# Optimization experiments

Hardware: AMD Instinct MI355X
Metric: run time of the kernel (lower is better)

The kernel has to match this reference:

```python
import jax, jax.numpy as jnp
import numpy as np

B, D, L, H = 256, 512, 64, 300


def setup_inputs() -> dict:
    key = jax.random.key(0)
    ks = jax.random.split(key, 16)
    s = 0.05  # weight init scale to keep activations sane through ReLU chains
    return {
        "x": jax.random.normal(ks[0], (B, D), jnp.float32),
        "eps": jax.random.normal(ks[1], (B, L), jnp.float32),
        "W": jax.random.normal(ks[2], (D, L), jnp.float32) * s,
        "enc1_w": jax.random.normal(ks[3], (H, D), jnp.float32) * s,
        "enc1_b": jax.random.normal(ks[4], (H,), jnp.float32) * s,
        "enc2_w": jax.random.normal(ks[5], (H, H), jnp.float32) * s,
        "enc2_b": jax.random.normal(ks[6], (H,), jnp.float32) * s,
        "zm_w": jax.random.normal(ks[7], (L, H), jnp.float32) * s,
        "zm_b": jax.random.normal(ks[8], (L,), jnp.float32) * s,
        "zv_w": jax.random.normal(ks[9], (L, H), jnp.float32) * s,
        "zv_b": jax.random.normal(ks[10], (L,), jnp.float32) * s,
        "gen1_w": jax.random.normal(ks[11], (H, L), jnp.float32) * s,
        "gen2_w": jax.random.normal(ks[12], (H, H), jnp.float32) * s,
        "gen2_b": jax.random.normal(ks[13], (H,), jnp.float32) * s,
        "head_w": jax.random.normal(ks[14], (D, H), jnp.float32) * s,
        "head_b": jax.random.normal(ks[15], (D,), jnp.float32) * s,
    }


def reference(x, eps, W, enc1_w, enc1_b, enc2_w, enc2_b, zm_w, zm_b,
              zv_w, zv_b, gen1_w, gen2_w, gen2_b, head_w, head_b):
    # encode: q_z = ReLU(Linear) -> ReLU(Linear)
    h = jax.nn.relu(x @ enc1_w.T + enc1_b)
    h = jax.nn.relu(h @ enc2_w.T + enc2_b)
    z_mean = h @ zm_w.T + zm_b          # [B, L]
    z_log_var = h @ zv_w.T + zv_b       # [B, L]
    # reparameterize (eps passed in for determinism)
    z = z_mean + eps * jnp.exp(0.5 * z_log_var)
    # decode: per-column masked z through shared generator + per-column head,
    # vectorized over the column axis D (mask = W rows)
    masked = z[:, None, :] * W[None, :, :]                       # [B, D, L]
    g1 = jax.nn.relu(jnp.einsum('bdl,hl->bdh', masked, gen1_w))  # [B, D, H]
    g2 = jax.nn.relu(jnp.einsum('bdh,gh->bdg', g1, gen2_w) + gen2_b)
    x_mean = jnp.einsum('bdh,dh->bd', g2, head_w) + head_b       # [B, D]
    return (x_mean, z, z_mean, z_log_var)
```

## Files before the change

### kernel.cpp

```cpp
#include <hip/hip_runtime.h>

typedef unsigned short u16;
typedef unsigned int u32;

typedef __bf16 bf16x8 __attribute__((ext_vector_type(8)));
typedef float f32x4 __attribute__((ext_vector_type(4)));

union V16 { uint4 u; bf16x8 v; u16 s[8]; __bf16 h[8]; };
union F4  { float4 v; float f[4]; };

__device__ __forceinline__ float bf2f(u16 a) {
  union { u32 u; float f; } c; c.u = ((u32)a) << 16; return c.f;
}

#define Z_OFF   131072
#define ZM_OFF  147456
#define ZLV_OFF 163840

#define B1_OFF 0
#define B2_OFF 2560
#define E1_OFF 15360
#define E2_OFF 35840
#define ZMP_OFF 48640
#define ZVP_OFF 51200
#define FRAG_TOTAL 53760
#define WB4  53760
#define XB4  57856
#define H1_4 74240
#define H2_4 84480
#define PACK_THREADS (FRAG_TOTAL + 4096 + 16384)

__device__ __forceinline__ void pack_one(const float* __restrict__ src,
                                         int t, int s, int lane,
                                         int Nsrc, int Ksrc, int rowlen,
                                         uint4* __restrict__ dst) {
  const int n = t * 16 + (lane & 15);
  const int k0 = s * 32 + ((lane >> 4) << 3);
  V16 v;
#pragma unroll
  for (int j = 0; j < 8; ++j) {
    const int k = k0 + j;
    v.h[j] = (n < Nsrc && k < Ksrc) ? (__bf16)src[n * rowlen + k] : (__bf16)0.f;
  }
  *dst = v.u;
}

__device__ __forceinline__ void cvt8(const float* __restrict__ src, uint4* __restrict__ dst) {
  F4 a, b; a.v = *(const float4*)src; b.v = *(const float4*)(src + 4);
  V16 v;
#pragma unroll
  for (int j = 0; j < 4; ++j) { v.h[j] = (__bf16)a.f[j]; v.h[4 + j] = (__bf16)b.f[j]; }
  *dst = v.u;
}

__global__ __launch_bounds__(256) void pack_kernel(
    const float* __restrict__ g1w, const float* __restrict__ g2w,
    const float* __restrict__ e1w, const float* __restrict__ e2w,
    const float* __restrict__ zmw, const float* __restrict__ zvw,
    const float* __restrict__ W,   const float* __restrict__ x,
    uint4* __restrict__ ws4) {
  const int idx = blockIdx.x * 256 + threadIdx.x;
  if (idx >= PACK_THREADS) return;
  const int lane = idx & 63;
  if (idx < B2_OFF) {
    const int f = (idx - B1_OFF) >> 6;
    pack_one(g1w, f >> 1, f & 1, lane, 300, 64, 64, ws4 + idx);
  } else if (idx < E1_OFF) {
    const int f = (idx - B2_OFF) >> 6;
    pack_one(g2w, f / 10, f % 10, lane, 300, 300, 300, ws4 + idx);
  } else if (idx < E2_OFF) {
    const int f = (idx - E1_OFF) >> 6;
    pack_one(e1w, f >> 4, f & 15, lane, 300, 512, 512, ws4 + idx);
  } else if (idx < ZMP_OFF) {
    const int f = (idx - E2_OFF) >> 6;
    pack_one(e2w, f / 10, f % 10, lane, 300, 300, 300, ws4 + idx);
  } else if (idx < ZVP_OFF) {
    const int f = (idx - ZMP_OFF) >> 6;
    pack_one(zmw, f / 10, f % 10, lane, 64, 300, 300, ws4 + idx);
  } else if (idx < FRAG_TOTAL) {
    const int f = (idx - ZVP_OFF) >> 6;
    pack_one(zvw, f / 10, f % 10, lane, 64, 300, 300, ws4 + idx);
  } else if (idx < FRAG_TOTAL + 4096) {
    const int i = idx - FRAG_TOTAL;
    cvt8(W + i * 8, ws4 + WB4 + i);
  } else {
    const int i = idx - FRAG_TOTAL - 4096;
    cvt8(x + i * 8, ws4 + XB4 + i);
  }
}

__global__ __launch_bounds__(64) void enc1_kernel(
    const uint4* __restrict__ xb, const uint4* __restrict__ e1p,
    const float* __restrict__ e1b, u16* __restrict__ h1) {
  const int wg = blockIdx.x;
  const int rt = wg / 20, nt = wg % 20;
  const int lane = threadIdx.x, q = lane >> 4, c = lane & 15;
  f32x4 acc = {0.f, 0.f, 0.f, 0.f};
  const int arow = rt * 16 + c;
#pragma unroll
  for (int s = 0; s < 16; ++s) {
    V16 a, b;
    a.u = xb[arow * 64 + s * 4 + q];
    b.u = e1p[(nt * 16 + s) * 64 + lane];
    acc = __builtin_amdgcn_mfma_f32_16x16x32_bf16(a.v, b.v, acc, 0, 0, 0);
  }
  const int col = nt * 16 + c;
  const float bias = (col < 300) ? e1b[col] : 0.f;
#pragma unroll
  for (int i = 0; i < 4; ++i) {
    const int row = rt * 16 + 4 * q + i;
    V16 t; t.h[0] = (col < 300) ? (__bf16)fmaxf(acc[i] + bias, 0.f) : (__bf16)0.f;
    h1[row * 320 + col] = t.s[0];
  }
}

__global__ __launch_bounds__(64) void enc2_kernel(
    const uint4* __restrict__ h1, const uint4* __restrict__ e2p,
    const float* __restrict__ e2b, u16* __restrict__ h2) {
  const int wg = blockIdx.x;
  const int rt = wg / 20, nt = wg % 20;
  const int lane = threadIdx.x, q = lane >> 4, c = lane & 15;
  f32x4 acc = {0.f, 0.f, 0.f, 0.f};
  const int arow = rt * 16 + c;
#pragma unroll
  for (int s = 0; s < 10; ++s) {
    V16 a, b;
    a.u = h1[arow * 40 + s * 4 + q];
    b.u = e2p[(nt * 10 + s) * 64 + lane];
    acc = __builtin_amdgcn_mfma_f32_16x16x32_bf16(a.v, b.v, acc, 0, 0, 0);
  }
  const int col = nt * 16 + c;
  const float bias = (col < 300) ? e2b[col] : 0.f;
#pragma unroll
  for (int i = 0; i < 4; ++i) {
    const int row = rt * 16 + 4 * q + i;
    V16 t; t.h[0] = (col < 300) ? (__bf16)fmaxf(acc[i] + bias, 0.f) : (__bf16)0.f;
    h2[row * 320 + col] = t.s[0];
  }
}

__global__ __launch_bounds__(64) void ench_kernel(
    const uint4* __restrict__ h2, const float* __restrict__ eps,
    const uint4* __restrict__ zmp, const float* __restrict__ zmb,
    const uint4* __restrict__ zvp, const float* __restrict__ zvb,
    float* __restrict__ out) {
  const int wg = blockIdx.x;
  const int rt = wg >> 2, t = wg & 3;
  const int lane = threadIdx.x, q = lane >> 4, c = lane & 15;
  f32x4 am = {0.f, 0.f, 0.f, 0.f}, av = {0.f, 0.f, 0.f, 0.f};
  const int arow = rt * 16 + c;
#pragma unroll
  for (int s = 0; s < 10; ++s) {
    V16 a, bm, bv;
    a.u = h2[arow * 40 + s * 4 + q];
    bm.u = zmp[(t * 10 + s) * 64 + lane];
    bv.u = zvp[(t * 10 + s) * 64 + lane];
    am = __builtin_amdgcn_mfma_f32_16x16x32_bf16(a.v, bm.v, am, 0, 0, 0);
    av = __builtin_amdgcn_mfma_f32_16x16x32_bf16(a.v, bv.v, av, 0, 0, 0);
  }
  const int col = t * 16 + c;
  const float bm = zmb[col], bv = zvb[col];
#pragma unroll
  for (int i = 0; i < 4; ++i) {
    const int gi = (rt * 16 + 4 * q + i) * 64 + col;
    const float zm = am[i] + bm;
    const float zlv = av[i] + bv;
    out[ZM_OFF + gi] = zm;
    out[ZLV_OFF + gi] = zlv;
    out[Z_OFF + gi] = zm + eps[gi] * expf(0.5f * zlv);
  }
}

__global__ __launch_bounds__(320, 4) void dec_kernel(
    const float* __restrict__ z,
    const uint4* __restrict__ Wb,
    const uint4* __restrict__ b1p,
    const uint4* __restrict__ b2p,
    const float* __restrict__ g2b,
    const float* __restrict__ hw,
    const float* __restrict__ hb,
    float* __restrict__ xout) {
  __shared__ u16 g1s[32 * 328];
  float* xredf = (float*)g1s;

  const int wg = blockIdx.x;
  const int r0 = wg << 5;
  const int bi = wg >> 4;
  const int d0 = r0 & 511;
  const int tid = threadIdx.x;
  const int u = tid >> 6;
  const int lane = tid & 63;
  const int q = lane >> 4;
  const int c = lane & 15;

  const float* zrow = z + bi * 64;

  bf16x8 bz[4][2];
#pragma unroll
  for (int kf = 0; kf < 2; ++kf) {
    F4 z0, z1;
    z0.v = *(const float4*)(zrow + kf * 32 + q * 8);
    z1.v = *(const float4*)(zrow + kf * 32 + q * 8 + 4);
#pragma unroll
    for (int tt = 0; tt < 4; ++tt) {
      V16 r; r.u = b1p[((4 * u + tt) * 2 + kf) * 64 + lane];
      V16 m;
#pragma unroll
      for (int j = 0; j < 4; ++j) {
        m.h[j]     = (__bf16)(bf2f(r.s[j])     * z0.f[j]);
        m.h[4 + j] = (__bf16)(bf2f(r.s[4 + j]) * z1.f[j]);
      }
      bz[tt][kf] = m.v;
    }
  }
#pragma unroll
  for (int rt = 0; rt < 2; ++rt) {
    const int rowA = rt * 16 + c;
    V16 af0, af1;
    af0.u = Wb[(d0 + rowA) * 8 + q];
    af1.u = Wb[(d0 + rowA) * 8 + 4 + q];
    f32x4 acc[4];
#pragma unroll
    for (int tt = 0; tt < 4; ++tt) acc[tt] = {0.f, 0.f, 0.f, 0.f};
#pragma unroll
    for (int tt = 0; tt < 4; ++tt) {
      acc[tt] = __builtin_amdgcn_mfma_f32_16x16x32_bf16(af0.v, bz[tt][0], acc[tt], 0, 0, 0);
      acc[tt] = __builtin_amdgcn_mfma_f32_16x16x32_bf16(af1.v, bz[tt][1], acc[tt], 0, 0, 0);
    }
    const int rwb = rt * 16 + 4 * q;
#pragma unroll
    for (int tt = 0; tt < 4; ++tt) {
      const int colb = (4 * u + tt) * 16 + c;
#pragma unroll
      for (int i = 0; i < 4; ++i) {
        V16 t; t.h[0] = (__bf16)fmaxf(acc[tt][i], 0.f);
        g1s[(rwb + i) * 328 + colb] = t.s[0];
      }
    }
  }
  __syncthreads();

  f32x4 a3[4][2];
#pragma unroll
  for (int tt = 0; tt < 4; ++tt)
#pragma unroll
    for (int rt = 0; rt < 2; ++rt) a3[tt][rt] = {0.f, 0.f, 0.f, 0.f};
  for (int s = 0; s < 10; ++s) {
    V16 b[4];
#pragma unroll
    for (int tt = 0; tt < 4; ++tt) b[tt].u = b2p[((4 * u + tt) * 10 + s) * 64 + lane];
#pragma unroll
    for (int rt = 0; rt < 2; ++rt) {
      V16 a; a.u = *(const uint4*)&g1s[(rt * 16 + c) * 328 + s * 32 + q * 8];
#pragma unroll
      for (int tt = 0; tt < 4; ++tt)
        a3[tt][rt] = __builtin_amdgcn_mfma_f32_16x16x32_bf16(a.v, b[tt].v, a3[tt][rt], 0, 0, 0);
    }
  }
  float xacc[2][4];
#pragma unroll
  for (int rt = 0; rt < 2; ++rt)
#pragma unroll
    for (int i = 0; i < 4; ++i) xacc[rt][i] = 0.f;
#pragma unroll
  for (int tt = 0; tt < 4; ++tt) {
    const int col = (4 * u + tt) * 16 + c;
    const bool inb = (col < 300);
    const float bias = inb ? g2b[col] : 0.f;
#pragma unroll
    for (int rt = 0; rt < 2; ++rt)
#pragma unroll
      for (int i = 0; i < 4; ++i) {
        const float g2v = fmaxf(a3[tt][rt][i] + bias, 0.f);
        const float h = inb ? hw[(d0 + rt * 16 + 4 * q + i) * 300 + col] : 0.f;
        xacc[rt][i] += g2v * h;
      }
  }
#pragma unroll
  for (int rt = 0; rt < 2; ++rt)
#pragma unroll
    for (int i = 0; i < 4; ++i) {
      float t = xacc[rt][i];
      t += __shfl_xor(t, 1);
      t += __shfl_xor(t, 2);
      t += __shfl_xor(t, 4);
      t += __shfl_xor(t, 8);
      xacc[rt][i] = t;
    }
  __syncthreads();
  if (c < 4) {
#pragma unroll
    for (int rt = 0; rt < 2; ++rt) {
      float t = xacc[rt][0];
      t = (c == 1) ? xacc[rt][1] : t;
      t = (c == 2) ? xacc[rt][2] : t;
      t = (c == 3) ? xacc[rt][3] : t;
      xredf[u * 32 + rt * 16 + 4 * q + c] = t;
    }
  }
  __syncthreads();
  if (tid < 32) {
    float t = hb[d0 + tid];
#pragma unroll
    for (int uu = 0; uu < 5; ++uu) t += xredf[uu * 32 + tid];
    xout[r0 + tid] = t;
  }
}

extern "C" void kernel_launch(void* const* d_in, const int* in_sizes, int n_in,
                              void* d_out, int out_size, void* d_ws, size_t ws_size,
                              hipStream_t stream) {
  const float* x   = (const float*)d_in[0];
  const float* eps = (const float*)d_in[1];
  const float* W   = (const float*)d_in[2];
  const float* e1w = (const float*)d_in[3];
  const float* e1b = (const float*)d_in[4];
  const float* e2w = (const float*)d_in[5];
  const float* e2b = (const float*)d_in[6];
  const float* zmw = (const float*)d_in[7];
  const float* zmb = (const float*)d_in[8];
  const float* zvw = (const float*)d_in[9];
  const float* zvb = (const float*)d_in[10];
  const float* g1w = (const float*)d_in[11];
  const float* g2w = (const float*)d_in[12];
  const float* g2b = (const float*)d_in[13];
  const float* hw  = (const float*)d_in[14];
  const float* hb  = (const float*)d_in[15];
  float* out = (float*)d_out;
  uint4* ws4 = (uint4*)d_ws;

  pack_kernel<<<(PACK_THREADS + 255) / 256, 256, 0, stream>>>(
      g1w, g2w, e1w, e2w, zmw, zvw, W, x, ws4);
  enc1_kernel<<<320, 64, 0, stream>>>(ws4 + XB4, ws4 + E1_OFF, e1b, (u16*)(ws4 + H1_4));
  enc2_kernel<<<320, 64, 0, stream>>>(ws4 + H1_4, ws4 + E2_OFF, e2b, (u16*)(ws4 + H2_4));
  ench_kernel<<<64, 64, 0, stream>>>(ws4 + H2_4, eps,
                                     ws4 + ZMP_OFF, zmb, ws4 + ZVP_OFF, zvb, out);
  dec_kernel<<<4096, 320, 0, stream>>>(out + Z_OFF, ws4 + WB4,
                                       ws4 + B1_OFF, ws4 + B2_OFF,
                                       g2b, hw, hb, out);
}
```

Before: 164.3 us.

## Fuse packing and encoder stages into one prep kernel; prefetch decoder B fragments

Merges the pack, enc1, enc2 and latent-head kernels into a single prep kernel. Sixteen workgroups run the whole encoder chain per 16-row batch tile, keeping h1/h2 in shared memory and converting weight fragments on the fly from fp32. The remaining workgroups pack only the decoder weights and W. In the decoder, gen2 B fragments are double-buffered and head weights are loaded before the MMA loop, with the occupancy hint lowered from 4 to 3 to make room for the extra registers. This removes three launches and the global round-trips for h1/h2, but encoder weights are now re-read and converted by each of the 16 workgroups, and the encoder runs on only 16 workgroups.

```diff
diff --git a/kernel.cpp b/kernel.cpp
--- a/kernel.cpp
+++ b/kernel.cpp
@@ -19,16 +19,10 @@
 
 #define B1_OFF 0
 #define B2_OFF 2560
-#define E1_OFF 15360
-#define E2_OFF 35840
-#define ZMP_OFF 48640
-#define ZVP_OFF 51200
-#define FRAG_TOTAL 53760
-#define WB4  53760
-#define XB4  57856
-#define H1_4 74240
-#define H2_4 84480
-#define PACK_THREADS (FRAG_TOTAL + 4096 + 16384)
+#define WB4    15360
+#define PACK_ITEMS 19456
+#define ENC_WGS 16
+#define PREP_WGS (ENC_WGS + PACK_ITEMS / 256)
 
 __device__ __forceinline__ void pack_one(const float* __restrict__ src,
                                          int t, int s, int lane,
@@ -53,116 +47,134 @@
   *dst = v.u;
 }
 
-__global__ __launch_bounds__(256) void pack_kernel(
+__device__ __forceinline__ bf16x8 bfrag(const float* __restrict__ src,
+                                        int n, int k0, int Nsrc, int Ksrc,
+                                        int rowlen) {
+  V16 m;
+  if (n < Nsrc && k0 + 8 <= Ksrc) {
+    F4 a, b;
+    a.v = *(const float4*)(src + n * rowlen + k0);
+    b.v = *(const float4*)(src + n * rowlen + k0 + 4);
+#pragma unroll
+    for (int j = 0; j < 4; ++j) { m.h[j] = (__bf16)a.f[j]; m.h[4 + j] = (__bf16)b.f[j]; }
+  } else if (n < Nsrc) {
+#pragma unroll
+    for (int j = 0; j < 8; ++j) {
+      const int k = k0 + j;
+      m.h[j] = (k < Ksrc) ? (__bf16)src[n * rowlen + k] : (__bf16)0.f;
+    }
+  } else {
+#pragma unroll
+    for (int j = 0; j < 8; ++j) m.h[j] = (__bf16)0.f;
+  }
+  return m.v;
+}
+
+__global__ __launch_bounds__(256, 2) void prep_kernel(
+    const float* __restrict__ x, const float* __restrict__ eps,
+    const float* __restrict__ e1w, const float* __restrict__ e1b,
+    const float* __restrict__ e2w, const float* __restrict__ e2b,
+    const float* __restrict__ zmw, const float* __restrict__ zmb,
+    const float* __restrict__ zvw, const float* __restrict__ zvb,
     const float* __restrict__ g1w, const float* __restrict__ g2w,
-    const float* __restrict__ e1w, const float* __restrict__ e2w,
-    const float* __restrict__ zmw, const float* __restrict__ zvw,
-    const float* __restrict__ W,   const float* __restrict__ x,
-    uint4* __restrict__ ws4) {
-  const int idx = blockIdx.x * 256 + threadIdx.x;
-  if (idx >= PACK_THREADS) return;
-  const int lane = idx & 63;
-  if (idx < B2_OFF) {
-    const int f = (idx - B1_OFF) >> 6;
-    pack_one(g1w, f >> 1, f & 1, lane, 300, 64, 64, ws4 + idx);
-  } else if (idx < E1_OFF) {
-    const int f = (idx - B2_OFF) >> 6;
-    pack_one(g2w, f / 10, f % 10, lane, 300, 300, 300, ws4 + idx);
-  } else if (idx < E2_OFF) {
-    const int f = (idx - E1_OFF) >> 6;
-    pack_one(e1w, f >> 4, f & 15, lane, 300, 512, 512, ws4 + idx);
-  } else if (idx < ZMP_OFF) {
-    const int f = (idx - E2_OFF) >> 6;
-    pack_one(e2w, f / 10, f % 10, lane, 300, 300, 300, ws4 + idx);
-  } else if (idx < ZVP_OFF) {
-    const int f = (idx - ZMP_OFF) >> 6;
-    pack_one(zmw, f / 10, f % 10, lane, 64, 300, 300, ws4 + idx);
-  } else if (idx < FRAG_TOTAL) {
-    const int f = (idx - ZVP_OFF) >> 6;
-    pack_one(zvw, f / 10, f % 10, lane, 64, 300, 300, ws4 + idx);
-  } else if (idx < FRAG_TOTAL + 4096) {
-    const int i = idx - FRAG_TOTAL;
-    cvt8(W + i * 8, ws4 + WB4 + i);
-  } else {
-    const int i = idx - FRAG_TOTAL - 4096;
-    cvt8(x + i * 8, ws4 + XB4 + i);
-  }
-}
-
-__global__ __launch_bounds__(64) void enc1_kernel(
-    const uint4* __restrict__ xb, const uint4* __restrict__ e1p,
-    const float* __restrict__ e1b, u16* __restrict__ h1) {
-  const int wg = blockIdx.x;
-  const int rt = wg / 20, nt = wg % 20;
-  const int lane = threadIdx.x, q = lane >> 4, c = lane & 15;
-  f32x4 acc = {0.f, 0.f, 0.f, 0.f};
-  const int arow = rt * 16 + c;
+    const float* __restrict__ W,
+    uint4* __restrict__ ws4, float* __restrict__ out) {
+  if (blockIdx.x >= ENC_WGS) {
+    const int idx = (blockIdx.x - ENC_WGS) * 256 + threadIdx.x;
+    const int lane = idx & 63;
+    if (idx < B2_OFF) {
+      const int f = idx >> 6;
+      pack_one(g1w, f >> 1, f & 1, lane, 300, 64, 64, ws4 + idx);
+    } else if (idx < WB4) {
+      const int f = (idx - B2_OFF) >> 6;
+      pack_one(g2w, f / 10, f % 10, lane, 300, 300, 300, ws4 + idx);
+    } else {
+      const int i = idx - WB4;
+      cvt8(W + i * 8, ws4 + WB4 + i);
+    }
+    return;
+  }
+
+  __shared__ u16 h1s[16 * 328];
+  __shared__ u16 h2s[16 * 328];
+  const int bi0 = blockIdx.x * 16;
+  const int tid = threadIdx.x;
+  const int w = tid >> 6, lane = tid & 63, q = lane >> 4, c = lane & 15;
+
+  bf16x8 af[16];
 #pragma unroll
   for (int s = 0; s < 16; ++s) {
-    V16 a, b;
-    a.u = xb[arow * 64 + s * 4 + q];
-    b.u = e1p[(nt * 16 + s) * 64 + lane];
-    acc = __builtin_amdgcn_mfma_f32_16x16x32_bf16(a.v, b.v, acc, 0, 0, 0);
-  }
-  const int col = nt * 16 + c;
-  const float bias = (col < 300) ? e1b[col] : 0.f;
+    const float* px = x + (bi0 + c) * 512 + s * 32 + q * 8;
+    F4 a, b; a.v = *(const float4*)px; b.v = *(const float4*)(px + 4);
+    V16 m;
+#pragma unroll
+    for (int j = 0; j < 4; ++j) { m.h[j] = (__bf16)a.f[j]; m.h[4 + j] = (__bf16)b.f[j]; }
+    af[s] = m.v;
+  }
+  f32x4 acc[5];
+#pragma unroll
+  for (int tt = 0; tt < 5; ++tt) acc[tt] = {0.f, 0.f, 0.f, 0.f};
+#pragma unroll
+  for (int s = 0; s < 16; ++s) {
+    const int k0 = s * 32 + q * 8;
+#pragma unroll
+    for (int tt = 0; tt < 5; ++tt) {
+      const int n = (w * 5 + tt) * 16 + c;
+      bf16x8 b = bfrag(e1w, n, k0, 300, 512, 512);
+      acc[tt] = __builtin_amdgcn_mfma_f32_16x16x32_bf16(af[s], b, acc[tt], 0, 0, 0);
+    }
+  }
+#pragma unroll
+  for (int tt = 0; tt < 5; ++tt) {
+    const int col = (w * 5 + tt) * 16 + c;
+    const float bias = (col < 300) ? e1b[col] : 0.f;
+#pragma unroll
+    for (int i = 0; i < 4; ++i) {
+      V16 t; t.h[0] = (col < 300) ? (__bf16)fmaxf(acc[tt][i] + bias, 0.f) : (__bf16)0.f;
+      h1s[(4 * q + i) * 328 + col] = t.s[0];
+    }
+  }
+  __syncthreads();
+#pragma unroll
+  for (int tt = 0; tt < 5; ++tt) acc[tt] = {0.f, 0.f, 0.f, 0.f};
+#pragma unroll
+  for (int s = 0; s < 10; ++s) {
+    V16 a; a.u = *(const uint4*)&h1s[c * 328 + s * 32 + q * 8];
+    const int k0 = s * 32 + q * 8;
+#pragma unroll
+    for (int tt = 0; tt < 5; ++tt) {
+      const int n = (w * 5 + tt) * 16 + c;
+      bf16x8 b = bfrag(e2w, n, k0, 300, 300, 300);
+      acc[tt] = __builtin_amdgcn_mfma_f32_16x16x32_bf16(a.v, b, acc[tt], 0, 0, 0);
+    }
+  }
+#pragma unroll
+  for (int tt = 0; tt < 5; ++tt) {
+    const int col = (w * 5 + tt) * 16 + c;
+    const float bias = (col < 300) ? e2b[col] : 0.f;
+#pragma unroll
+    for (int i = 0; i < 4; ++i) {
+      V16 t; t.h[0] = (col < 300) ? (__bf16)fmaxf(acc[tt][i] + bias, 0.f) : (__bf16)0.f;
+      h2s[(4 * q + i) * 328 + col] = t.s[0];
+    }
+  }
+  __syncthreads();
+  f32x4 am = {0.f, 0.f, 0.f, 0.f}, av = {0.f, 0.f, 0.f, 0.f};
+#pragma unroll
+  for (int s = 0; s < 10; ++s) {
+    V16 a; a.u = *(const uint4*)&h2s[c * 328 + s * 32 + q * 8];
+    const int k0 = s * 32 + q * 8;
+    const int n = w * 16 + c;
+    bf16x8 bm = bfrag(zmw, n, k0, 64, 300, 300);
+    bf16x8 bv = bfrag(zvw, n, k0, 64, 300, 300);
+    am = __builtin_amdgcn_mfma_f32_16x16x32_bf16(a.v, bm, am, 0, 0, 0);
+    av = __builtin_amdgcn_mfma_f32_16x16x32_bf16(a.v, bv, av, 0, 0, 0);
+  }
+  const int col = w * 16 + c;
+  const float bm = zmb[col], bv = zvb[col];
 #pragma unroll
   for (int i = 0; i < 4; ++i) {
-    const int row = rt * 16 + 4 * q + i;
-    V16 t; t.h[0] = (col < 300) ? (__bf16)fmaxf(acc[i] + bias, 0.f) : (__bf16)0.f;
-    h1[row * 320 + col] = t.s[0];
-  }
-}
-
-__global__ __launch_bounds__(64) void enc2_kernel(
-    const uint4* __restrict__ h1, const uint4* __restrict__ e2p,
-    const float* __restrict__ e2b, u16* __restrict__ h2) {
-  const int wg = blockIdx.x;
-  const int rt = wg / 20, nt = wg % 20;
-  const int lane = threadIdx.x, q = lane >> 4, c = lane & 15;
-  f32x4 acc = {0.f, 0.f, 0.f, 0.f};
-  const int arow = rt * 16 + c;
-#pragma unroll
-  for (int s = 0; s < 10; ++s) {
-    V16 a, b;
-    a.u = h1[arow * 40 + s * 4 + q];
-    b.u = e2p[(nt * 10 + s) * 64 + lane];
-    acc = __builtin_amdgcn_mfma_f32_16x16x32_bf16(a.v, b.v, acc, 0, 0, 0);
-  }
-  const int col = nt * 16 + c;
-  const float bias = (col < 300) ? e2b[col] : 0.f;
-#pragma unroll
-  for (int i = 0; i < 4; ++i) {
-    const int row = rt * 16 + 4 * q + i;
-    V16 t; t.h[0] = (col < 300) ? (__bf16)fmaxf(acc[i] + bias, 0.f) : (__bf16)0.f;
-    h2[row * 320 + col] = t.s[0];
-  }
-}
-
-__global__ __launch_bounds__(64) void ench_kernel(
-    const uint4* __restrict__ h2, const float* __restrict__ eps,
-    const uint4* __restrict__ zmp, const float* __restrict__ zmb,
-    const uint4* __restrict__ zvp, const float* __restrict__ zvb,
-    float* __restrict__ out) {
-  const int wg = blockIdx.x;
-  const int rt = wg >> 2, t = wg & 3;
-  const int lane = threadIdx.x, q = lane >> 4, c = lane & 15;
-  f32x4 am = {0.f, 0.f, 0.f, 0.f}, av = {0.f, 0.f, 0.f, 0.f};
-  const int arow = rt * 16 + c;
-#pragma unroll
-  for (int s = 0; s < 10; ++s) {
-    V16 a, bm, bv;
-    a.u = h2[arow * 40 + s * 4 + q];
-    bm.u = zmp[(t * 10 + s) * 64 + lane];
-    bv.u = zvp[(t * 10 + s) * 64 + lane];
-    am = __builtin_amdgcn_mfma_f32_16x16x32_bf16(a.v, bm.v, am, 0, 0, 0);
-    av = __builtin_amdgcn_mfma_f32_16x16x32_bf16(a.v, bv.v, av, 0, 0, 0);
-  }
-  const int col = t * 16 + c;
-  const float bm = zmb[col], bv = zvb[col];
-#pragma unroll
-  for (int i = 0; i < 4; ++i) {
-    const int gi = (rt * 16 + 4 * q + i) * 64 + col;
+    const int gi = (bi0 + 4 * q + i) * 64 + col;
     const float zm = am[i] + bm;
     const float zlv = av[i] + bv;
     out[ZM_OFF + gi] = zm;
@@ -171,7 +183,7 @@
   }
 }
 
-__global__ __launch_bounds__(320, 4) void dec_kernel(
+__global__ __launch_bounds__(320, 3) void dec_kernel(
     const float* __restrict__ z,
     const uint4* __restrict__ Wb,
     const uint4* __restrict__ b1p,
@@ -240,42 +252,57 @@
   }
   __syncthreads();
 
-  f32x4 a3[4][2];
-#pragma unroll
-  for (int tt = 0; tt < 4; ++tt)
-#pragma unroll
-    for (int rt = 0; rt < 2; ++rt) a3[tt][rt] = {0.f, 0.f, 0.f, 0.f};
-  for (int s = 0; s < 10; ++s) {
-    V16 b[4];
-#pragma unroll
-    for (int tt = 0; tt < 4; ++tt) b[tt].u = b2p[((4 * u + tt) * 10 + s) * 64 + lane];
-#pragma unroll
-    for (int rt = 0; rt < 2; ++rt) {
-      V16 a; a.u = *(const uint4*)&g1s[(rt * 16 + c) * 328 + s * 32 + q * 8];
-#pragma unroll
-      for (int tt = 0; tt < 4; ++tt)
-        a3[tt][rt] = __builtin_amdgcn_mfma_f32_16x16x32_bf16(a.v, b[tt].v, a3[tt][rt], 0, 0, 0);
-    }
-  }
-  float xacc[2][4];
-#pragma unroll
-  for (int rt = 0; rt < 2; ++rt)
-#pragma unroll
-    for (int i = 0; i < 4; ++i) xacc[rt][i] = 0.f;
+  float hwv[4][2][4];
+  float bias[4];
 #pragma unroll
   for (int tt = 0; tt < 4; ++tt) {
     const int col = (4 * u + tt) * 16 + c;
     const bool inb = (col < 300);
-    const float bias = inb ? g2b[col] : 0.f;
+    bias[tt] = inb ? g2b[col] : 0.f;
 #pragma unroll
     for (int rt = 0; rt < 2; ++rt)
 #pragma unroll
-      for (int i = 0; i < 4; ++i) {
-        const float g2v = fmaxf(a3[tt][rt][i] + bias, 0.f);
-        const float h = inb ? hw[(d0 + rt * 16 + 4 * q + i) * 300 + col] : 0.f;
-        xacc[rt][i] += g2v * h;
-      }
-  }
+      for (int i = 0; i < 4; ++i)
+        hwv[tt][rt][i] = inb ? hw[(d0 + rt * 16 + 4 * q + i) * 300 + col] : 0.f;
+  }
+
+  f32x4 a3[4][2];
+#pragma unroll
+  for (int tt = 0; tt < 4; ++tt)
+#pragma unroll
+    for (int rt = 0; rt < 2; ++rt) a3[tt][rt] = {0.f, 0.f, 0.f, 0.f};
+  V16 bp[2][4];
+#pragma unroll
+  for (int tt = 0; tt < 4; ++tt) bp[0][tt].u = b2p[((4 * u + tt) * 10 + 0) * 64 + lane];
+  for (int s = 0; s < 10; ++s) {
+    const int cur = s & 1, nxt = cur ^ 1;
+    if (s < 9) {
+#pragma unroll
+      for (int tt = 0; tt < 4; ++tt)
+        bp[nxt][tt].u = b2p[((4 * u + tt) * 10 + s + 1) * 64 + lane];
+    }
+#pragma unroll
+    for (int rt = 0; rt < 2; ++rt) {
+      V16 a; a.u = *(const uint4*)&g1s[(rt * 16 + c) * 328 + s * 32 + q * 8];
+#pragma unroll
+      for (int tt = 0; tt < 4; ++tt)
+        a3[tt][rt] = __builtin_amdgcn_mfma_f32_16x16x32_bf16(a.v, bp[cur][tt].v, a3[tt][rt], 0, 0, 0);
+    }
+  }
+
+  float xacc[2][4];
+#pragma unroll
+  for (int rt = 0; rt < 2; ++rt)
+#pragma unroll
+    for (int i = 0; i < 4; ++i) xacc[rt][i] = 0.f;
+#pragma unroll
+  for (int tt = 0; tt < 4; ++tt)
+#pragma unroll
+    for (int rt = 0; rt < 2; ++rt)
+#pragma unroll
+      for (int i = 0; i < 4; ++i)
+        xacc[rt][i] += fmaxf(a3[tt][rt][i] + bias[tt], 0.f) * hwv[tt][rt][i];
+
 #pragma unroll
   for (int rt = 0; rt < 2; ++rt)
 #pragma unroll
@@ -329,12 +356,9 @@
   float* out = (float*)d_out;
   uint4* ws4 = (uint4*)d_ws;
 
-  pack_kernel<<<(PACK_THREADS + 255) / 256, 256, 0, stream>>>(
-      g1w, g2w, e1w, e2w, zmw, zvw, W, x, ws4);
-  enc1_kernel<<<320, 64, 0, stream>>>(ws4 + XB4, ws4 + E1_OFF, e1b, (u16*)(ws4 + H1_4));
-  enc2_kernel<<<320, 64, 0, stream>>>(ws4 + H1_4, ws4 + E2_OFF, e2b, (u16*)(ws4 + H2_4));
-  ench_kernel<<<64, 64, 0, stream>>>(ws4 + H2_4, eps,
-                                     ws4 + ZMP_OFF, zmb, ws4 + ZVP_OFF, zvb, out);
+  prep_kernel<<<PREP_WGS, 256, 0, stream>>>(x, eps, e1w, e1b, e2w, e2b,
+                                            zmw, zmb, zvw, zvb, g1w, g2w, W,
+                                            ws4, out);
   dec_kernel<<<4096, 320, 0, stream>>>(out + Z_OFF, ws4 + WB4,
                                        ws4 + B1_OFF, ws4 + B2_OFF,
                                        g2b, hw, hb, out);
```

New measurement: 221.4 us. +34.8%, slower.

## Fuse all stages into one persistent kernel with software grid barriers

Applied to the files above, without the earlier changes.

Replaces the five separate launches (pack, enc1, enc2, latent head, decoder) with one persistent kernel of 512 workgroups. Stages are separated by an atomic-counter grid barrier, and the decoder loops over its 4096 tiles. The goal is to remove launch gaps and tail effects between the small encoder kernels. In exchange the grid must be fully co-resident for the spin barrier to avoid deadlock, a memset is added each call, and the small stages now run on only a fraction of the grid while the rest wait.

```diff
diff --git a/kernel.cpp b/kernel.cpp
--- a/kernel.cpp
+++ b/kernel.cpp
@@ -28,7 +28,10 @@
 #define XB4  57856
 #define H1_4 74240
 #define H2_4 84480
-#define PACK_THREADS (FRAG_TOTAL + 4096 + 16384)
+#define PACK_ITEMS 74240
+#define BAR_U4 94720
+#define NWG 512
+#define NTHR 320
 
 __device__ __forceinline__ void pack_one(const float* __restrict__ src,
                                          int t, int s, int lane,
@@ -53,257 +56,277 @@
   *dst = v.u;
 }
 
-__global__ __launch_bounds__(256) void pack_kernel(
+__device__ __forceinline__ void gbar(u32* bar, u32 target, int tid) {
+  __syncthreads();
+  if (tid == 0) {
+    __threadfence();
+    __hip_atomic_fetch_add(bar, 1u, __ATOMIC_RELEASE, __HIP_MEMORY_SCOPE_AGENT);
+    u32 v;
+    do {
+      __builtin_amdgcn_s_sleep(4);
+      v = __hip_atomic_load(bar, __ATOMIC_ACQUIRE, __HIP_MEMORY_SCOPE_AGENT);
+    } while (v < target);
+  }
+  __syncthreads();
+}
+
+__global__ __launch_bounds__(NTHR, 4) void fused_kernel(
+    const float* __restrict__ x, const float* __restrict__ eps,
+    const float* __restrict__ e1w, const float* __restrict__ e1b,
+    const float* __restrict__ e2w, const float* __restrict__ e2b,
+    const float* __restrict__ zmw, const float* __restrict__ zmb,
+    const float* __restrict__ zvw, const float* __restrict__ zvb,
     const float* __restrict__ g1w, const float* __restrict__ g2w,
-    const float* __restrict__ e1w, const float* __restrict__ e2w,
-    const float* __restrict__ zmw, const float* __restrict__ zvw,
-    const float* __restrict__ W,   const float* __restrict__ x,
-    uint4* __restrict__ ws4) {
-  const int idx = blockIdx.x * 256 + threadIdx.x;
-  if (idx >= PACK_THREADS) return;
-  const int lane = idx & 63;
-  if (idx < B2_OFF) {
-    const int f = (idx - B1_OFF) >> 6;
-    pack_one(g1w, f >> 1, f & 1, lane, 300, 64, 64, ws4 + idx);
-  } else if (idx < E1_OFF) {
-    const int f = (idx - B2_OFF) >> 6;
-    pack_one(g2w, f / 10, f % 10, lane, 300, 300, 300, ws4 + idx);
-  } else if (idx < E2_OFF) {
-    const int f = (idx - E1_OFF) >> 6;
-    pack_one(e1w, f >> 4, f & 15, lane, 300, 512, 512, ws4 + idx);
-  } else if (idx < ZMP_OFF) {
-    const int f = (idx - E2_OFF) >> 6;
-    pack_one(e2w, f / 10, f % 10, lane, 300, 300, 300, ws4 + idx);
-  } else if (idx < ZVP_OFF) {
-    const int f = (idx - ZMP_OFF) >> 6;
-    pack_one(zmw, f / 10, f % 10, lane, 64, 300, 300, ws4 + idx);
-  } else if (idx < FRAG_TOTAL) {
-    const int f = (idx - ZVP_OFF) >> 6;
-    pack_one(zvw, f / 10, f % 10, lane, 64, 300, 300, ws4 + idx);
-  } else if (idx < FRAG_TOTAL + 4096) {
-    const int i = idx - FRAG_TOTAL;
-    cvt8(W + i * 8, ws4 + WB4 + i);
-  } else {
-    const int i = idx - FRAG_TOTAL - 4096;
-    cvt8(x + i * 8, ws4 + XB4 + i);
-  }
-}
-
-__global__ __launch_bounds__(64) void enc1_kernel(
-    const uint4* __restrict__ xb, const uint4* __restrict__ e1p,
-    const float* __restrict__ e1b, u16* __restrict__ h1) {
-  const int wg = blockIdx.x;
-  const int rt = wg / 20, nt = wg % 20;
-  const int lane = threadIdx.x, q = lane >> 4, c = lane & 15;
-  f32x4 acc = {0.f, 0.f, 0.f, 0.f};
-  const int arow = rt * 16 + c;
-#pragma unroll
-  for (int s = 0; s < 16; ++s) {
-    V16 a, b;
-    a.u = xb[arow * 64 + s * 4 + q];
-    b.u = e1p[(nt * 16 + s) * 64 + lane];
-    acc = __builtin_amdgcn_mfma_f32_16x16x32_bf16(a.v, b.v, acc, 0, 0, 0);
-  }
-  const int col = nt * 16 + c;
-  const float bias = (col < 300) ? e1b[col] : 0.f;
-#pragma unroll
-  for (int i = 0; i < 4; ++i) {
-    const int row = rt * 16 + 4 * q + i;
-    V16 t; t.h[0] = (col < 300) ? (__bf16)fmaxf(acc[i] + bias, 0.f) : (__bf16)0.f;
-    h1[row * 320 + col] = t.s[0];
-  }
-}
-
-__global__ __launch_bounds__(64) void enc2_kernel(
-    const uint4* __restrict__ h1, const uint4* __restrict__ e2p,
-    const float* __restrict__ e2b, u16* __restrict__ h2) {
-  const int wg = blockIdx.x;
-  const int rt = wg / 20, nt = wg % 20;
-  const int lane = threadIdx.x, q = lane >> 4, c = lane & 15;
-  f32x4 acc = {0.f, 0.f, 0.f, 0.f};
-  const int arow = rt * 16 + c;
-#pragma unroll
-  for (int s = 0; s < 10; ++s) {
-    V16 a, b;
-    a.u = h1[arow * 40 + s * 4 + q];
-    b.u = e2p[(nt * 10 + s) * 64 + lane];
-    acc = __builtin_amdgcn_mfma_f32_16x16x32_bf16(a.v, b.v, acc, 0, 0, 0);
-  }
-  const int col = nt * 16 + c;
-  const float bias = (col < 300) ? e2b[col] : 0.f;
-#pragma unroll
-  for (int i = 0; i < 4; ++i) {
-    const int row = rt * 16 + 4 * q + i;
-    V16 t; t.h[0] = (col < 300) ? (__bf16)fmaxf(acc[i] + bias, 0.f) : (__bf16)0.f;
-    h2[row * 320 + col] = t.s[0];
-  }
-}
-
-__global__ __launch_bounds__(64) void ench_kernel(
-    const uint4* __restrict__ h2, const float* __restrict__ eps,
-    const uint4* __restrict__ zmp, const float* __restrict__ zmb,
-    const uint4* __restrict__ zvp, const float* __restrict__ zvb,
-    float* __restrict__ out) {
-  const int wg = blockIdx.x;
-  const int rt = wg >> 2, t = wg & 3;
-  const int lane = threadIdx.x, q = lane >> 4, c = lane & 15;
-  f32x4 am = {0.f, 0.f, 0.f, 0.f}, av = {0.f, 0.f, 0.f, 0.f};
-  const int arow = rt * 16 + c;
-#pragma unroll
-  for (int s = 0; s < 10; ++s) {
-    V16 a, bm, bv;
-    a.u = h2[arow * 40 + s * 4 + q];
-    bm.u = zmp[(t * 10 + s) * 64 + lane];
-    bv.u = zvp[(t * 10 + s) * 64 + lane];
-    am = __builtin_amdgcn_mfma_f32_16x16x32_bf16(a.v, bm.v, am, 0, 0, 0);
-    av = __builtin_amdgcn_mfma_f32_16x16x32_bf16(a.v, bv.v, av, 0, 0, 0);
-  }
-  const int col = t * 16 + c;
-  const float bm = zmb[col], bv = zvb[col];
-#pragma unroll
-  for (int i = 0; i < 4; ++i) {
-    const int gi = (rt * 16 + 4 * q + i) * 64 + col;
-    const float zm = am[i] + bm;
-    const float zlv = av[i] + bv;
-    out[ZM_OFF + gi] = zm;
-    out[ZLV_OFF + gi] = zlv;
-    out[Z_OFF + gi] = zm + eps[gi] * expf(0.5f * zlv);
-  }
-}
-
-__global__ __launch_bounds__(320, 4) void dec_kernel(
-    const float* __restrict__ z,
-    const uint4* __restrict__ Wb,
-    const uint4* __restrict__ b1p,
-    const uint4* __restrict__ b2p,
-    const float* __restrict__ g2b,
-    const float* __restrict__ hw,
-    const float* __restrict__ hb,
-    float* __restrict__ xout) {
+    const float* __restrict__ g2b, const float* __restrict__ hw,
+    const float* __restrict__ hb, const float* __restrict__ W,
+    uint4* __restrict__ ws4, float* __restrict__ out) {
   __shared__ u16 g1s[32 * 328];
   float* xredf = (float*)g1s;
 
-  const int wg = blockIdx.x;
-  const int r0 = wg << 5;
-  const int bi = wg >> 4;
-  const int d0 = r0 & 511;
+  u32* bar = (u32*)(ws4 + BAR_U4);
+  const int wgid = blockIdx.x;
   const int tid = threadIdx.x;
-  const int u = tid >> 6;
   const int lane = tid & 63;
   const int q = lane >> 4;
   const int c = lane & 15;
-
-  const float* zrow = z + bi * 64;
-
-  bf16x8 bz[4][2];
-#pragma unroll
-  for (int kf = 0; kf < 2; ++kf) {
-    F4 z0, z1;
-    z0.v = *(const float4*)(zrow + kf * 32 + q * 8);
-    z1.v = *(const float4*)(zrow + kf * 32 + q * 8 + 4);
+  const int gw = wgid * 5 + (tid >> 6);
+
+  {
+    const int idx = wgid * NTHR + tid;
+    if (idx < PACK_ITEMS) {
+      const int l = idx & 63;
+      if (idx < B2_OFF) {
+        const int f = idx >> 6;
+        pack_one(g1w, f >> 1, f & 1, l, 300, 64, 64, ws4 + idx);
+      } else if (idx < E1_OFF) {
+        const int f = (idx - B2_OFF) >> 6;
+        pack_one(g2w, f / 10, f % 10, l, 300, 300, 300, ws4 + idx);
+      } else if (idx < E2_OFF) {
+        const int f = (idx - E1_OFF) >> 6;
+        pack_one(e1w, f >> 4, f & 15, l, 300, 512, 512, ws4 + idx);
+      } else if (idx < ZMP_OFF) {
+        const int f = (idx - E2_OFF) >> 6;
+        pack_one(e2w, f / 10, f % 10, l, 300, 300, 300, ws4 + idx);
+      } else if (idx < ZVP_OFF) {
+        const int f = (idx - ZMP_OFF) >> 6;
+        pack_one(zmw, f / 10, f % 10, l, 64, 300, 300, ws4 + idx);
+      } else if (idx < FRAG_TOTAL) {
+        const int f = (idx - ZVP_OFF) >> 6;
+        pack_one(zvw, f / 10, f % 10, l, 64, 300, 300, ws4 + idx);
+      } else if (idx < XB4) {
+        const int i = idx - WB4;
+        cvt8(W + i * 8, ws4 + WB4 + i);
+      } else {
+        const int i = idx - XB4;
+        cvt8(x + i * 8, ws4 + XB4 + i);
+      }
+    }
+  }
+  gbar(bar, 1 * NWG, tid);
+
+  if (gw < 320) {
+    const uint4* xb = ws4 + XB4;
+    const uint4* e1p = ws4 + E1_OFF;
+    u16* h1 = (u16*)(ws4 + H1_4);
+    const int rt = gw / 20, nt = gw % 20;
+    f32x4 acc = {0.f, 0.f, 0.f, 0.f};
+    const int arow = rt * 16 + c;
+#pragma unroll
+    for (int s = 0; s < 16; ++s) {
+      V16 a, b;
+      a.u = xb[arow * 64 + s * 4 + q];
+      b.u = e1p[(nt * 16 + s) * 64 + lane];
+      acc = __builtin_amdgcn_mfma_f32_16x16x32_bf16(a.v, b.v, acc, 0, 0, 0);
+    }
+    const int col = nt * 16 + c;
+    const float bias = (col < 300) ? e1b[col] : 0.f;
+#pragma unroll
+    for (int i = 0; i < 4; ++i) {
+      const int row = rt * 16 + 4 * q + i;
+      V16 t; t.h[0] = (col < 300) ? (__bf16)fmaxf(acc[i] + bias, 0.f) : (__bf16)0.f;
+      h1[row * 320 + col] = t.s[0];
+    }
+  }
+  gbar(bar, 2 * NWG, tid);
+
+  if (gw < 320) {
+    const uint4* h1 = ws4 + H1_4;
+    const uint4* e2p = ws4 + E2_OFF;
+    u16* h2 = (u16*)(ws4 + H2_4);
+    const int rt = gw / 20, nt = gw % 20;
+    f32x4 acc = {0.f, 0.f, 0.f, 0.f};
+    const int arow = rt * 16 + c;
+#pragma unroll
+    for (int s = 0; s < 10; ++s) {
+      V16 a, b;
+      a.u = h1[arow * 40 + s * 4 + q];
+      b.u = e2p[(nt * 10 + s) * 64 + lane];
+      acc = __builtin_amdgcn_mfma_f32_16x16x32_bf16(a.v, b.v, acc, 0, 0, 0);
+    }
+    const int col = nt * 16 + c;
+    const float bias = (col < 300) ? e2b[col] : 0.f;
+#pragma unroll
+    for (int i = 0; i < 4; ++i) {
+      const int row = rt * 16 + 4 * q + i;
+      V16 t; t.h[0] = (col < 300) ? (__bf16)fmaxf(acc[i] + bias, 0.f) : (__bf16)0.f;
+      h2[row * 320 + col] = t.s[0];
+    }
+  }
+  gbar(bar, 3 * NWG, tid);
+
+  if (gw < 64) {
+    const uint4* h2 = ws4 + H2_4;
+    const uint4* zmp = ws4 + ZMP_OFF;
+    const uint4* zvp = ws4 + ZVP_OFF;
+    const int rt = gw >> 2, t = gw & 3;
+    f32x4 am = {0.f, 0.f, 0.f, 0.f}, av = {0.f, 0.f, 0.f, 0.f};
+    const int arow = rt * 16 + c;
+#pragma unroll
+    for (int s = 0; s < 10; ++s) {
+      V16 a, bm, bv;
+      a.u = h2[arow * 40 + s * 4 + q];
+      bm.u = zmp[(t * 10 + s) * 64 + lane];
+      bv.u = zvp[(t * 10 + s) * 64 + lane];
+      am = __builtin_amdgcn_mfma_f32_16x16x32_bf16(a.v, bm.v, am, 0, 0, 0);
+      av = __builtin_amdgcn_mfma_f32_16x16x32_bf16(a.v, bv.v, av, 0, 0, 0);
+    }
+    const int col = t * 16 + c;
+    const float bm = zmb[col], bv = zvb[col];
+#pragma unroll
+    for (int i = 0; i < 4; ++i) {
+      const int gi = (rt * 16 + 4 * q + i) * 64 + col;
+      const float zm = am[i] + bm;
+      const float zlv = av[i] + bv;
+      out[ZM_OFF + gi] = zm;
+      out[ZLV_OFF + gi] = zlv;
+      out[Z_OFF + gi] = zm + eps[gi] * expf(0.5f * zlv);
+    }
+  }
+  gbar(bar, 4 * NWG, tid);
+
+  const float* z = out + Z_OFF;
+  const uint4* Wb = ws4 + WB4;
+  const uint4* b1p = ws4 + B1_OFF;
+  const uint4* b2p = ws4 + B2_OFF;
+  const int u = tid >> 6;
+
+  for (int vt = wgid; vt < 4096; vt += NWG) {
+    const int r0 = vt << 5;
+    const int bi = vt >> 4;
+    const int d0 = r0 & 511;
+    const float* zrow = z + bi * 64;
+
+    bf16x8 bz[4][2];
+#pragma unroll
+    for (int kf = 0; kf < 2; ++kf) {
+      F4 z0, z1;
+      z0.v = *(const float4*)(zrow + kf * 32 + q * 8);
+      z1.v = *(const float4*)(zrow + kf * 32 + q * 8 + 4);
+#pragma unroll
+      for (int tt = 0; tt < 4; ++tt) {
+        V16 r; r.u = b1p[((4 * u + tt) * 2 + kf) * 64 + lane];
+        V16 m;
+#pragma unroll
+        for (int j = 0; j < 4; ++j) {
+          m.h[j]     = (__bf16)(bf2f(r.s[j])     * z0.f[j]);
+          m.h[4 + j] = (__bf16)(bf2f(r.s[4 + j]) * z1.f[j]);
+        }
+        bz[tt][kf] = m.v;
+      }
+    }
+#pragma unroll
+    for (int rt = 0; rt < 2; ++rt) {
+      const int rowA = rt * 16 + c;
+      V16 af0, af1;
+      af0.u = Wb[(d0 + rowA) * 8 + q];
+      af1.u = Wb[(d0 + rowA) * 8 + 4 + q];
+      f32x4 acc[4];
+#pragma unroll
+      for (int tt = 0; tt < 4; ++tt) acc[tt] = {0.f, 0.f, 0.f, 0.f};
+#pragma unroll
+      for (int tt = 0; tt < 4; ++tt) {
+        acc[tt] = __builtin_amdgcn_mfma_f32_16x16x32_bf16(af0.v, bz[tt][0], acc[tt], 0, 0, 0);
+        acc[tt] = __builtin_amdgcn_mfma_f32_16x16x32_bf16(af1.v, bz[tt][1], acc[tt], 0, 0, 0);
+      }
+      const int rwb = rt * 16 + 4 * q;
+#pragma unroll
+      for (int tt = 0; tt < 4; ++tt) {
+        const int colb = (4 * u + tt) * 16 + c;
+#pragma unroll
+        for (int i = 0; i < 4; ++i) {
+          V16 t; t.h[0] = (__bf16)fmaxf(acc[tt][i], 0.f);
+          g1s[(rwb + i) * 328 + colb] = t.s[0];
+        }
+      }
+    }
+    __syncthreads();
+
+    f32x4 a3[4][2];
+#pragma unroll
+    for (int tt = 0; tt < 4; ++tt)
+#pragma unroll
+      for (int rt = 0; rt < 2; ++rt) a3[tt][rt] = {0.f, 0.f, 0.f, 0.f};
+    for (int s = 0; s < 10; ++s) {
+      V16 b[4];
+#pragma unroll
+      for (int tt = 0; tt < 4; ++tt) b[tt].u = b2p[((4 * u + tt) * 10 + s) * 64 + lane];
+#pragma unroll
+      for (int rt = 0; rt < 2; ++rt) {
+        V16 a; a.u = *(const uint4*)&g1s[(rt * 16 + c) * 328 + s * 32 + q * 8];
+#pragma unroll
+        for (int tt = 0; tt < 4; ++tt)
+          a3[tt][rt] = __builtin_amdgcn_mfma_f32_16x16x32_bf16(a.v, b[tt].v, a3[tt][rt], 0, 0, 0);
+      }
+    }
+    float xacc[2][4];
+#pragma unroll
+    for (int rt = 0; rt < 2; ++rt)
+#pragma unroll
+      for (int i = 0; i < 4; ++i) xacc[rt][i] = 0.f;
 #pragma unroll
     for (int tt = 0; tt < 4; ++tt) {
-      V16 r; r.u = b1p[((4 * u + tt) * 2 + kf) * 64 + lane];
-      V16 m;
-#pragma unroll
-      for (int j = 0; j < 4; ++j) {
-        m.h[j]     = (__bf16)(bf2f(r.s[j])     * z0.f[j]);
-        m.h[4 + j] = (__bf16)(bf2f(r.s[4 + j]) * z1.f[j]);
-      }
-      bz[tt][kf] = m.v;
-    }
-  }
-#pragma unroll
-  for (int rt = 0; rt < 2; ++rt) {
-    const int rowA = rt * 16 + c;
-    V16 af0, af1;
-    af0.u = Wb[(d0 + rowA) * 8 + q];
-    af1.u = Wb[(d0 + rowA) * 8 + 4 + q];
-    f32x4 acc[4];
-#pragma unroll
-    for (int tt = 0; tt < 4; ++tt) acc[tt] = {0.f, 0.f, 0.f, 0.f};
-#pragma unroll
-    for (int tt = 0; tt < 4; ++tt) {
-      acc[tt] = __builtin_amdgcn_mfma_f32_16x16x32_bf16(af0.v, bz[tt][0], acc[tt], 0, 0, 0);
-      acc[tt] = __builtin_amdgcn_mfma_f32_16x16x32_bf16(af1.v, bz[tt][1], acc[tt], 0, 0, 0);
-    }
-    const int rwb = rt * 16 + 4 * q;
-#pragma unroll
-    for (int tt = 0; tt < 4; ++tt) {
-      const int colb = (4 * u + tt) * 16 + c;
+      const int col = (4 * u + tt) * 16 + c;
+      const bool inb = (col < 300);
+      const float bias = inb ? g2b[col] : 0.f;
+#pragma unroll
+      for (int rt = 0; rt < 2; ++rt)
+#pragma unroll
+        for (int i = 0; i < 4; ++i) {
+          const float g2v = fmaxf(a3[tt][rt][i] + bias, 0.f);
+          const float h = inb ? hw[(d0 + rt * 16 + 4 * q + i) * 300 + col] : 0.f;
+          xacc[rt][i] += g2v * h;
+        }
+    }
+#pragma unroll
+    for (int rt = 0; rt < 2; ++rt)
 #pragma unroll
       for (int i = 0; i < 4; ++i) {
-        V16 t; t.h[0] = (__bf16)fmaxf(acc[tt][i], 0.f);
-        g1s[(rwb + i) * 328 + colb] = t.s[0];
-      }
-    }
-  }
-  __syncthreads();
-
-  f32x4 a3[4][2];
-#pragma unroll
-  for (int tt = 0; tt < 4; ++tt)
-#pragma unroll
-    for (int rt = 0; rt < 2; ++rt) a3[tt][rt] = {0.f, 0.f, 0.f, 0.f};
-  for (int s = 0; s < 10; ++s) {
-    V16 b[4];
-#pragma unroll
-    for (int tt = 0; tt < 4; ++tt) b[tt].u = b2p[((4 * u + tt) * 10 + s) * 64 + lane];
-#pragma unroll
-    for (int rt = 0; rt < 2; ++rt) {
-      V16 a; a.u = *(const uint4*)&g1s[(rt * 16 + c) * 328 + s * 32 + q * 8];
-#pragma unroll
-      for (int tt = 0; tt < 4; ++tt)
-        a3[tt][rt] = __builtin_amdgcn_mfma_f32_16x16x32_bf16(a.v, b[tt].v, a3[tt][rt], 0, 0, 0);
-    }
-  }
-  float xacc[2][4];
-#pragma unroll
-  for (int rt = 0; rt < 2; ++rt)
-#pragma unroll
-    for (int i = 0; i < 4; ++i) xacc[rt][i] = 0.f;
-#pragma unroll
-  for (int tt = 0; tt < 4; ++tt) {
-    const int col = (4 * u + tt) * 16 + c;
-    const bool inb = (col < 300);
-    const float bias = inb ? g2b[col] : 0.f;
-#pragma unroll
-    for (int rt = 0; rt < 2; ++rt)
-#pragma unroll
-      for (int i = 0; i < 4; ++i) {
-        const float g2v = fmaxf(a3[tt][rt][i] + bias, 0.f);
-        const float h = inb ? hw[(d0 + rt * 16 + 4 * q + i) * 300 + col] : 0.f;
-        xacc[rt][i] += g2v * h;
-      }
-  }
-#pragma unroll
-  for (int rt = 0; rt < 2; ++rt)
-#pragma unroll
-    for (int i = 0; i < 4; ++i) {
-      float t = xacc[rt][i];
-      t += __shfl_xor(t, 1);
-      t += __shfl_xor(t, 2);
-      t += __shfl_xor(t, 4);
-      t += __shfl_xor(t, 8);
-      xacc[rt][i] = t;
-    }
-  __syncthreads();
-  if (c < 4) {
-#pragma unroll
-    for (int rt = 0; rt < 2; ++rt) {
-      float t = xacc[rt][0];
-      t = (c == 1) ? xacc[rt][1] : t;
-      t = (c == 2) ? xacc[rt][2] : t;
-      t = (c == 3) ? xacc[rt][3] : t;
-      xredf[u * 32 + rt * 16 + 4 * q + c] = t;
-    }
-  }
-  __syncthreads();
-  if (tid < 32) {
-    float t = hb[d0 + tid];
-#pragma unroll
-    for (int uu = 0; uu < 5; ++uu) t += xredf[uu * 32 + tid];
-    xout[r0 + tid] = t;
+        float t = xacc[rt][i];
+        t += __shfl_xor(t, 1);
+        t += __shfl_xor(t, 2);
+        t += __shfl_xor(t, 4);
+        t += __shfl_xor(t, 8);
+        xacc[rt][i] = t;
+      }
+    __syncthreads();
+    if (c < 4) {
+#pragma unroll
+      for (int rt = 0; rt < 2; ++rt) {
+        float t = xacc[rt][0];
+        t = (c == 1) ? xacc[rt][1] : t;
+        t = (c == 2) ? xacc[rt][2] : t;
+        t = (c == 3) ? xacc[rt][3] : t;
+        xredf[u * 32 + rt * 16 + 4 * q + c] = t;
+      }
+    }
+    __syncthreads();
+    if (tid < 32) {
+      float t = hb[d0 + tid];
+#pragma unroll
+      for (int uu = 0; uu < 5; ++uu) t += xredf[uu * 32 + tid];
+      out[r0 + tid] = t;
+    }
+    __syncthreads();
   }
 }
 
@@ -329,13 +352,8 @@
   float* out = (float*)d_out;
   uint4* ws4 = (uint4*)d_ws;
 
-  pack_kernel<<<(PACK_THREADS + 255) / 256, 256, 0, stream>>>(
-      g1w, g2w, e1w, e2w, zmw, zvw, W, x, ws4);
-  enc1_kernel<<<320, 64, 0, stream>>>(ws4 + XB4, ws4 + E1_OFF, e1b, (u16*)(ws4 + H1_4));
-  enc2_kernel<<<320, 64, 0, stream>>>(ws4 + H1_4, ws4 + E2_OFF, e2b, (u16*)(ws4 + H2_4));
-  ench_kernel<<<64, 64, 0, stream>>>(ws4 + H2_4, eps,
-                                     ws4 + ZMP_OFF, zmb, ws4 + ZVP_OFF, zvb, out);
-  dec_kernel<<<4096, 320, 0, stream>>>(out + Z_OFF, ws4 + WB4,
-                                       ws4 + B1_OFF, ws4 + B2_OFF,
-                                       g2b, hw, hb, out);
-}
+  hipMemsetAsync((char*)d_ws + (size_t)BAR_U4 * 16, 0, 4, stream);
+  fused_kernel<<<NWG, NTHR, 0, stream>>>(x, eps, e1w, e1b, e2w, e2b,
+                                         zmw, zmb, zvw, zvb, g1w, g2w,
+                                         g2b, hw, hb, W, ws4, out);
+}
```

After: 471.8 us. 2.87x slower.
